# Optimization experiments

Hardware: AMD Instinct MI355X
Metric: run time of the kernel (lower is better)

The kernel has to match this reference:

```python
import jax, jax.numpy as jnp
import numpy as np

D_IN = 1024
D_OUT = 1024
N_HEADS = 16
HEAD_DIM = D_OUT // N_HEADS


def setup_inputs() -> dict:
    key = jax.random.key(0)
    ks = jax.random.split(key, 5)
    scale = 0.02
    x = jax.random.normal(ks[0], (2, 2048, D_IN), dtype=jnp.float32)
    Wq = jax.random.normal(ks[1], (D_IN, D_OUT), dtype=jnp.float32) * scale
    Wk = jax.random.normal(ks[2], (D_IN, D_OUT), dtype=jnp.float32) * scale
    Wv = jax.random.normal(ks[3], (D_IN, D_OUT), dtype=jnp.float32) * scale
    Wout = jax.random.normal(ks[4], (D_OUT, D_OUT), dtype=jnp.float32) * scale
    return {"x": x, "Wq": Wq, "Wk": Wk, "Wv": Wv, "Wout": Wout}


def reference(x, Wq, Wk, Wv, Wout):
    batch, seq_len, _ = x.shape
    # projections (no bias)
    Q = (x @ Wq).reshape(batch, seq_len, N_HEADS, HEAD_DIM)
    K = (x @ Wk).reshape(batch, seq_len, N_HEADS, HEAD_DIM)
    V = (x @ Wv).reshape(batch, seq_len, N_HEADS, HEAD_DIM)
    # scores: [batch, heads, seq, seq]
    scores = jnp.einsum("bqhd,bkhd->bhqk", Q, K) / jnp.sqrt(
        jnp.asarray(HEAD_DIM, dtype=x.dtype)
    )
    # causal mask: positions k > q masked to -inf
    causal = jnp.tril(jnp.ones((seq_len, seq_len), dtype=bool))
    scores = jnp.where(causal[None, None], scores, -jnp.inf)
    weights = jax.nn.softmax(scores, axis=-1)
    vectors = jnp.einsum("bhqk,bkhd->bqhd", weights, V)
    vectors = vectors.reshape(batch, seq_len, D_OUT)
    return vectors @ Wout
```

## Files before the change

### kernel.cpp

```cpp
#include <hip/hip_runtime.h>
#include <hip/hip_bf16.h>


typedef __attribute__((ext_vector_type(8))) _Float16 vhalf8;
typedef __attribute__((ext_vector_type(4))) _Float16 vhalf4;
typedef __attribute__((ext_vector_type(4))) float vfloat4;

#define D_MODEL 1024
#define SEQ     2048
#define NB      2
#define NH      16
#define HD      64

#define SCALE_K1 0.18033688f

__device__ __forceinline__ void async16(const void* g, void* l) {
  __builtin_amdgcn_global_load_lds(
      (const __attribute__((address_space(1))) unsigned int*)g,
      (__attribute__((address_space(3))) unsigned int*)l, 16, 0, 0);
}

__global__ __launch_bounds__(256) void prep(
    const float* __restrict__ x,
    const float* __restrict__ Wq, const float* __restrict__ Wk,
    const float* __restrict__ Wv, const float* __restrict__ Wo,
    _Float16* __restrict__ Xh, _Float16* __restrict__ Wt_qkv,
    _Float16* __restrict__ Wot) {
  int z = blockIdx.z;
  int t = threadIdx.x;
  if (z == 4) {
    int id = blockIdx.y * 16 + blockIdx.x;
#pragma unroll
    for (int pass = 0; pass < 8; pass++) {
      size_t i = ((size_t)(pass * 256 + id) * 256 + t) * 8;
      float4 a = *(const float4*)&x[i];
      float4 b = *(const float4*)&x[i + 4];
      vhalf8 h;
      h[0] = (_Float16)a.x; h[1] = (_Float16)a.y;
      h[2] = (_Float16)a.z; h[3] = (_Float16)a.w;
      h[4] = (_Float16)b.x; h[5] = (_Float16)b.y;
      h[6] = (_Float16)b.z; h[7] = (_Float16)b.w;
      *(vhalf8*)&Xh[i] = h;
    }
    return;
  }
  __shared__ _Float16 tile[64][65];
  const float* in = (z == 0) ? Wq : (z == 1) ? Wk : (z == 2) ? Wv : Wo;
  _Float16* out = (z < 3) ? (Wt_qkv + (size_t)z * 1024 * 1024) : Wot;
  int c0 = blockIdx.x * 64, r0 = blockIdx.y * 64;
  int tc = t & 63, tr = t >> 6;
#pragma unroll
  for (int p = 0; p < 16; p++) {
    int r = tr + p * 4;
    tile[r][tc] = (_Float16)in[(size_t)(r0 + r) * 1024 + c0 + tc];
  }
  __syncthreads();
#pragma unroll
  for (int p = 0; p < 16; p++) {
    int r = tr + p * 4;
    out[(size_t)(c0 + r) * 1024 + r0 + tc] = tile[tc][r];
  }
}

template <int BN>
__global__ __launch_bounds__(256) void gemm128(
    const _Float16* __restrict__ A, const _Float16* __restrict__ Bt,
    _Float16* __restrict__ Ch, float* __restrict__ Cf,
    _Float16* __restrict__ Vt, int M, int N, int K, int mode) {
  constexpr int NC = 8 + BN / 16;
  constexpr int CPW = NC / 4;
  constexpr int JN = BN / 32;
  __shared__ _Float16 As[128 * 32];
  __shared__ _Float16 Bs[BN * 32];
  int m0 = blockIdx.x * 128, n0 = blockIdx.y * BN;
  int t = threadIdx.x;
  int lane = t & 63, wave = t >> 6;
  int wm = (wave >> 1) * 64, wn = (wave & 1) * (BN / 2);
  int col = lane & 15, quad = lane >> 4;
  int srow = lane >> 2;
  int skc = (lane & 3) << 3;

  vfloat4 acc[4][JN];
#pragma unroll
  for (int i = 0; i < 4; i++)
#pragma unroll
    for (int j = 0; j < JN; j++) {
      acc[i][j][0] = 0.f; acc[i][j][1] = 0.f;
      acc[i][j][2] = 0.f; acc[i][j][3] = 0.f;
    }

  for (int k0 = 0; k0 < K; k0 += 32) {
    __syncthreads();
#pragma unroll
    for (int j = 0; j < CPW; j++) {
      int c = wave * CPW + j;
      int row = ((c < 8) ? c : (c - 8)) * 16 + srow;
      if (c < 8)
        async16(&A[(size_t)(m0 + row) * K + k0 + skc], &As[c * 512]);
      else
        async16(&Bt[(size_t)(n0 + row) * K + k0 + skc], &Bs[(c - 8) * 512]);
    }
    __syncthreads();

    vhalf8 af[4], bf[JN];
#pragma unroll
    for (int i = 0; i < 4; i++)
      af[i] = *(const vhalf8*)&As[(wm + i * 16 + col) * 32 + quad * 8];
#pragma unroll
    for (int j = 0; j < JN; j++)
      bf[j] = *(const vhalf8*)&Bs[(wn + j * 16 + col) * 32 + quad * 8];
#pragma unroll
    for (int i = 0; i < 4; i++)
#pragma unroll
      for (int j = 0; j < JN; j++)
        acc[i][j] = __builtin_amdgcn_mfma_f32_16x16x32_f16(af[i], bf[j], acc[i][j], 0, 0, 0);
  }

  bool vmode = (mode == 2) && (n0 >= 2048);
#pragma unroll
  for (int i = 0; i < 4; i++)
#pragma unroll
    for (int j = 0; j < JN; j++)
#pragma unroll
      for (int r = 0; r < 4; r++) {
        int m = m0 + wm + i * 16 + quad * 4 + r;
        int n = n0 + wn + j * 16 + col;
        if (mode == 1) {
          Cf[(size_t)m * N + n] = acc[i][j][r];
        } else if (vmode) {
          int nn = n - 2048;
          int hh = nn >> 6, dd = nn & 63;
          int bb = m >> 11, ss = m & 2047;
          Vt[(((size_t)bb * NH + hh) * HD + dd) * SEQ + ss] = (_Float16)acc[i][j][r];
        } else {
          Ch[(size_t)m * N + n] = (_Float16)acc[i][j][r];
        }
      }
}

__global__ __launch_bounds__(512) void attn(
    const _Float16* __restrict__ QKV, const _Float16* __restrict__ Vt,
    _Float16* __restrict__ Vec) {
  int blk = blockIdx.x;
  int qt = 15 - (blk >> 5);
  int hb = blk & 31;
  int h = hb & 15;
  int b = hb >> 4;
  int q0 = qt * 128;

  const _Float16* Qb  = QKV + (size_t)(b * SEQ) * 3072 + h * HD;
  const _Float16* Kb  = QKV + (size_t)(b * SEQ) * 3072 + 1024 + h * HD;
  const _Float16* Vtb = Vt + (size_t)(b * NH + h) * HD * SEQ;

  int t = threadIdx.x;
  int lane = t & 63, wave = t >> 6;
  int col = lane & 15, quad = lane >> 4;
  int wq0 = q0 + wave * 16;

  __shared__ _Float16 Ks[64][72];
  __shared__ _Float16 Vs[64][72];
  __shared__ _Float16 Ps[8][16][72];

  vhalf8 qf0 = *(const vhalf8*)&Qb[(size_t)(wq0 + col) * 3072 + quad * 8];
  vhalf8 qf1 = *(const vhalf8*)&Qb[(size_t)(wq0 + col) * 3072 + 32 + quad * 8];
#pragma unroll
  for (int i = 0; i < 8; i++) {
    qf0[i] = qf0[i] * (_Float16)SCALE_K1;
    qf1[i] = qf1[i] * (_Float16)SCALE_K1;
  }

  vfloat4 o[4];
#pragma unroll
  for (int i = 0; i < 4; i++) { o[i][0]=0.f; o[i][1]=0.f; o[i][2]=0.f; o[i][3]=0.f; }
  float lsum[4] = {0.f, 0.f, 0.f, 0.f};

  int srow = t >> 3;
  int scol = (t & 7) * 8;
  int kslot = ((srow & 3) << 4) + (srow >> 2);
  int kcol = scol ^ ((srow & 3) << 4);

  vhalf8 kr, vr;
  kr = *(const vhalf8*)&Kb[(size_t)srow * 3072 + scol];
  vr = *(const vhalf8*)&Vtb[(size_t)srow * SEQ + scol];

  for (int kb = 0; kb <= q0 + 127; kb += 64) {
    *(vhalf8*)&Ks[kslot][kcol] = kr;
    *(vhalf8*)&Vs[srow][scol]  = vr;
    __syncthreads();

    if (kb < q0 + 64) {
      kr = *(const vhalf8*)&Kb[(size_t)(kb + 64 + srow) * 3072 + scol];
      vr = *(const vhalf8*)&Vtb[(size_t)srow * SEQ + kb + 64 + scol];
    }

    if (kb <= wq0 + 15) {
      vfloat4 s[4];
#pragma unroll
      for (int hh = 0; hh < 4; hh++) {
        int sw = hh << 4;
        vhalf8 kf0 = *(const vhalf8*)&Ks[hh * 16 + col][(quad * 8) ^ sw];
        vhalf8 kf1 = *(const vhalf8*)&Ks[hh * 16 + col][(32 + quad * 8) ^ sw];
        vfloat4 z; z[0]=0.f; z[1]=0.f; z[2]=0.f; z[3]=0.f;
        z = __builtin_amdgcn_mfma_f32_16x16x32_f16(qf0, kf0, z, 0, 0, 0);
        z = __builtin_amdgcn_mfma_f32_16x16x32_f16(qf1, kf1, z, 0, 0, 0);
        s[hh] = z;
      }
      bool diag = (kb + 63 > wq0);
#pragma unroll
      for (int r = 0; r < 4; r++) {
        int q = wq0 + quad * 4 + r;
        float p[4];
#pragma unroll
        for (int hh = 0; hh < 4; hh++) {
          float sc = s[hh][r];
          if (diag && (kb + 4 * col + hh > q)) sc = -1e30f;
          p[hh] = __builtin_exp2f(sc);
        }
        lsum[r] += (p[0] + p[1]) + (p[2] + p[3]);
        vhalf4 ph;
        ph[0] = (_Float16)p[0]; ph[1] = (_Float16)p[1];
        ph[2] = (_Float16)p[2]; ph[3] = (_Float16)p[3];
        *(vhalf4*)&Ps[wave][quad * 4 + r][4 * col] = ph;
      }
      __asm__ __volatile__("s_waitcnt lgkmcnt(0)" ::: "memory");
      vhalf8 pf0 = *(const vhalf8*)&Ps[wave][col][quad * 8];
      vhalf8 pf1 = *(const vhalf8*)&Ps[wave][col][32 + quad * 8];
#pragma unroll
      for (int tt = 0; tt < 4; tt++) {
        vhalf8 vf0 = *(const vhalf8*)&Vs[tt * 16 + col][quad * 8];
        vhalf8 vf1 = *(const vhalf8*)&Vs[tt * 16 + col][32 + quad * 8];
        o[tt] = __builtin_amdgcn_mfma_f32_16x16x32_f16(pf0, vf0, o[tt], 0, 0, 0);
        o[tt] = __builtin_amdgcn_mfma_f32_16x16x32_f16(pf1, vf1, o[tt], 0, 0, 0);
      }
    }
    __syncthreads();
  }

  float inv_l[4];
#pragma unroll
  for (int r = 0; r < 4; r++) {
    float rs = lsum[r];
#pragma unroll
    for (int msk = 1; msk < 16; msk <<= 1) rs += __shfl_xor(rs, msk, 64);
    inv_l[r] = 1.0f / rs;
  }
#pragma unroll
  for (int tt = 0; tt < 4; tt++)
#pragma unroll
    for (int r = 0; r < 4; r++) {
      int q = wq0 + quad * 4 + r;
      int d = tt * 16 + col;
      Vec[(size_t)(b * SEQ + q) * D_MODEL + h * HD + d] =
          (_Float16)(o[tt][r] * inv_l[r]);
    }
}

extern "C" void kernel_launch(void* const* d_in, const int* in_sizes, int n_in,
                              void* d_out, int out_size, void* d_ws, size_t ws_size,
                              hipStream_t stream) {
  const float* x  = (const float*)d_in[0];
  const float* Wq = (const float*)d_in[1];
  const float* Wk = (const float*)d_in[2];
  const float* Wv = (const float*)d_in[3];
  const float* Wo = (const float*)d_in[4];
  float* out = (float*)d_out;

  char* ws = (char*)d_ws;
  _Float16* Xh     = (_Float16*)ws;
  _Float16* Wt_qkv = (_Float16*)(ws + 8388608);
  _Float16* Wot    = (_Float16*)(ws + 14680064);
  _Float16* QKV    = (_Float16*)(ws + 16777216);
  _Float16* Vt     = (_Float16*)(ws + 41943040);
  _Float16* Vec    = (_Float16*)(ws + 50331648);

  dim3 tb(256);
  prep<<<dim3(16, 16, 5), tb, 0, stream>>>(x, Wq, Wk, Wv, Wo, Xh, Wt_qkv, Wot);
  gemm128<128><<<dim3(32, 24), tb, 0, stream>>>(Xh, Wt_qkv, QKV, nullptr, Vt,
                                                4096, 3072, 1024, 2);
  attn<<<dim3(512), dim3(512), 0, stream>>>(QKV, Vt, Vec);
  gemm128<64><<<dim3(32, 16), tb, 0, stream>>>(Vec, Wot, nullptr, out, nullptr,
                                               4096, 1024, 1024, 1);
}
```

Measured before the change: 193.1 us.

## Double GEMM K-tile and give each attention wave two query groups

The GEMM kernel is templated on BK and now stages 64-wide K slices into shared memory, halving the number of barrier pairs per K loop. The attention kernel drops to 256 threads, with each wave handling 32 query rows as two 16-row groups. Each K/V fragment read from shared memory is reused across both groups, and each thread loads twice as many K/V elements per tile. The query-tile order is changed to interleave long and short causal tiles for load balance, at the cost of more registers per thread and fewer waves per block.

```diff
diff --git a/kernel.cpp b/kernel.cpp
--- a/kernel.cpp
+++ b/kernel.cpp
@@ -62,23 +62,26 @@
   }
 }
 
-template <int BN>
+template <int BN, int BK>
 __global__ __launch_bounds__(256) void gemm128(
     const _Float16* __restrict__ A, const _Float16* __restrict__ Bt,
     _Float16* __restrict__ Ch, float* __restrict__ Cf,
     _Float16* __restrict__ Vt, int M, int N, int K, int mode) {
-  constexpr int NC = 8 + BN / 16;
-  constexpr int CPW = NC / 4;
+  constexpr int ACH = 128 * BK / 512;
+  constexpr int BCH = BN * BK / 512;
+  constexpr int CPW = (ACH + BCH) / 4;
+  constexpr int RPC = 512 / BK;
+  constexpr int LPR = BK / 8;
   constexpr int JN = BN / 32;
-  __shared__ _Float16 As[128 * 32];
-  __shared__ _Float16 Bs[BN * 32];
+  __shared__ _Float16 As[128 * BK];
+  __shared__ _Float16 Bs[BN * BK];
   int m0 = blockIdx.x * 128, n0 = blockIdx.y * BN;
   int t = threadIdx.x;
   int lane = t & 63, wave = t >> 6;
   int wm = (wave >> 1) * 64, wn = (wave & 1) * (BN / 2);
   int col = lane & 15, quad = lane >> 4;
-  int srow = lane >> 2;
-  int skc = (lane & 3) << 3;
+  int srow = lane / LPR;
+  int skc = (lane % LPR) * 8;
 
   vfloat4 acc[4][JN];
 #pragma unroll
@@ -89,31 +92,36 @@
       acc[i][j][2] = 0.f; acc[i][j][3] = 0.f;
     }
 
-  for (int k0 = 0; k0 < K; k0 += 32) {
+  for (int k0 = 0; k0 < K; k0 += BK) {
     __syncthreads();
 #pragma unroll
     for (int j = 0; j < CPW; j++) {
       int c = wave * CPW + j;
-      int row = ((c < 8) ? c : (c - 8)) * 16 + srow;
-      if (c < 8)
+      if (c < ACH) {
+        int row = c * RPC + srow;
         async16(&A[(size_t)(m0 + row) * K + k0 + skc], &As[c * 512]);
-      else
-        async16(&Bt[(size_t)(n0 + row) * K + k0 + skc], &Bs[(c - 8) * 512]);
+      } else {
+        int row = (c - ACH) * RPC + srow;
+        async16(&Bt[(size_t)(n0 + row) * K + k0 + skc], &Bs[(c - ACH) * 512]);
+      }
     }
     __syncthreads();
 
-    vhalf8 af[4], bf[JN];
-#pragma unroll
-    for (int i = 0; i < 4; i++)
-      af[i] = *(const vhalf8*)&As[(wm + i * 16 + col) * 32 + quad * 8];
-#pragma unroll
-    for (int j = 0; j < JN; j++)
-      bf[j] = *(const vhalf8*)&Bs[(wn + j * 16 + col) * 32 + quad * 8];
-#pragma unroll
-    for (int i = 0; i < 4; i++)
+#pragma unroll
+    for (int sub = 0; sub < BK / 32; sub++) {
+      vhalf8 af[4], bf[JN];
+#pragma unroll
+      for (int i = 0; i < 4; i++)
+        af[i] = *(const vhalf8*)&As[(wm + i * 16 + col) * BK + sub * 32 + quad * 8];
 #pragma unroll
       for (int j = 0; j < JN; j++)
-        acc[i][j] = __builtin_amdgcn_mfma_f32_16x16x32_f16(af[i], bf[j], acc[i][j], 0, 0, 0);
+        bf[j] = *(const vhalf8*)&Bs[(wn + j * 16 + col) * BK + sub * 32 + quad * 8];
+#pragma unroll
+      for (int i = 0; i < 4; i++)
+#pragma unroll
+        for (int j = 0; j < JN; j++)
+          acc[i][j] = __builtin_amdgcn_mfma_f32_16x16x32_f16(af[i], bf[j], acc[i][j], 0, 0, 0);
+    }
   }
 
   bool vmode = (mode == 2) && (n0 >= 2048);
@@ -138,11 +146,12 @@
       }
 }
 
-__global__ __launch_bounds__(512) void attn(
+__global__ __launch_bounds__(256) void attn(
     const _Float16* __restrict__ QKV, const _Float16* __restrict__ Vt,
     _Float16* __restrict__ Vec) {
   int blk = blockIdx.x;
-  int qt = 15 - (blk >> 5);
+  int j = blk >> 5;
+  int qt = (j < 8) ? (15 - j) : (j - 8);
   int hb = blk & 31;
   int h = hb & 15;
   int b = hb >> 4;
@@ -155,104 +164,137 @@
   int t = threadIdx.x;
   int lane = t & 63, wave = t >> 6;
   int col = lane & 15, quad = lane >> 4;
-  int wq0 = q0 + wave * 16;
+  int wq0 = q0 + wave * 32;
 
   __shared__ _Float16 Ks[64][72];
   __shared__ _Float16 Vs[64][72];
-  __shared__ _Float16 Ps[8][16][72];
-
-  vhalf8 qf0 = *(const vhalf8*)&Qb[(size_t)(wq0 + col) * 3072 + quad * 8];
-  vhalf8 qf1 = *(const vhalf8*)&Qb[(size_t)(wq0 + col) * 3072 + 32 + quad * 8];
-#pragma unroll
-  for (int i = 0; i < 8; i++) {
-    qf0[i] = qf0[i] * (_Float16)SCALE_K1;
-    qf1[i] = qf1[i] * (_Float16)SCALE_K1;
-  }
-
-  vfloat4 o[4];
-#pragma unroll
-  for (int i = 0; i < 4; i++) { o[i][0]=0.f; o[i][1]=0.f; o[i][2]=0.f; o[i][3]=0.f; }
-  float lsum[4] = {0.f, 0.f, 0.f, 0.f};
-
-  int srow = t >> 3;
-  int scol = (t & 7) * 8;
+  __shared__ _Float16 Ps[4][32][72];
+
+  vhalf8 qf[2][2];
+#pragma unroll
+  for (int g = 0; g < 2; g++) {
+    qf[g][0] = *(const vhalf8*)&Qb[(size_t)(wq0 + g * 16 + col) * 3072 + quad * 8];
+    qf[g][1] = *(const vhalf8*)&Qb[(size_t)(wq0 + g * 16 + col) * 3072 + 32 + quad * 8];
+#pragma unroll
+    for (int i = 0; i < 8; i++) {
+      qf[g][0][i] = qf[g][0][i] * (_Float16)SCALE_K1;
+      qf[g][1][i] = qf[g][1][i] * (_Float16)SCALE_K1;
+    }
+  }
+
+  vfloat4 o[2][4];
+#pragma unroll
+  for (int g = 0; g < 2; g++)
+#pragma unroll
+    for (int i = 0; i < 4; i++) {
+      o[g][i][0] = 0.f; o[g][i][1] = 0.f; o[g][i][2] = 0.f; o[g][i][3] = 0.f;
+    }
+  float lsum[2][4] = {{0.f, 0.f, 0.f, 0.f}, {0.f, 0.f, 0.f, 0.f}};
+
+  int srow = t >> 2;
+  int scol = (t & 3) * 16;
   int kslot = ((srow & 3) << 4) + (srow >> 2);
   int kcol = scol ^ ((srow & 3) << 4);
 
-  vhalf8 kr, vr;
-  kr = *(const vhalf8*)&Kb[(size_t)srow * 3072 + scol];
-  vr = *(const vhalf8*)&Vtb[(size_t)srow * SEQ + scol];
+  vhalf8 kr0, kr1, vr0, vr1;
+  {
+    const _Float16* kg = &Kb[(size_t)srow * 3072 + scol];
+    kr0 = *(const vhalf8*)kg; kr1 = *(const vhalf8*)(kg + 8);
+    const _Float16* vg = &Vtb[(size_t)srow * SEQ + scol];
+    vr0 = *(const vhalf8*)vg; vr1 = *(const vhalf8*)(vg + 8);
+  }
 
   for (int kb = 0; kb <= q0 + 127; kb += 64) {
-    *(vhalf8*)&Ks[kslot][kcol] = kr;
-    *(vhalf8*)&Vs[srow][scol]  = vr;
+    *(vhalf8*)&Ks[kslot][kcol]     = kr0;
+    *(vhalf8*)&Ks[kslot][kcol + 8] = kr1;
+    *(vhalf8*)&Vs[srow][scol]      = vr0;
+    *(vhalf8*)&Vs[srow][scol + 8]  = vr1;
     __syncthreads();
 
     if (kb < q0 + 64) {
-      kr = *(const vhalf8*)&Kb[(size_t)(kb + 64 + srow) * 3072 + scol];
-      vr = *(const vhalf8*)&Vtb[(size_t)srow * SEQ + kb + 64 + scol];
-    }
-
-    if (kb <= wq0 + 15) {
-      vfloat4 s[4];
+      const _Float16* kg = &Kb[(size_t)(kb + 64 + srow) * 3072 + scol];
+      kr0 = *(const vhalf8*)kg; kr1 = *(const vhalf8*)(kg + 8);
+      const _Float16* vg = &Vtb[(size_t)srow * SEQ + kb + 64 + scol];
+      vr0 = *(const vhalf8*)vg; vr1 = *(const vhalf8*)(vg + 8);
+    }
+
+    if (kb <= wq0 + 31) {
+      vhalf8 kf[4][2];
 #pragma unroll
       for (int hh = 0; hh < 4; hh++) {
         int sw = hh << 4;
-        vhalf8 kf0 = *(const vhalf8*)&Ks[hh * 16 + col][(quad * 8) ^ sw];
-        vhalf8 kf1 = *(const vhalf8*)&Ks[hh * 16 + col][(32 + quad * 8) ^ sw];
-        vfloat4 z; z[0]=0.f; z[1]=0.f; z[2]=0.f; z[3]=0.f;
-        z = __builtin_amdgcn_mfma_f32_16x16x32_f16(qf0, kf0, z, 0, 0, 0);
-        z = __builtin_amdgcn_mfma_f32_16x16x32_f16(qf1, kf1, z, 0, 0, 0);
-        s[hh] = z;
-      }
-      bool diag = (kb + 63 > wq0);
+        kf[hh][0] = *(const vhalf8*)&Ks[hh * 16 + col][(quad * 8) ^ sw];
+        kf[hh][1] = *(const vhalf8*)&Ks[hh * 16 + col][(32 + quad * 8) ^ sw];
+      }
+#pragma unroll
+      for (int g = 0; g < 2; g++) {
+        vfloat4 s[4];
+#pragma unroll
+        for (int hh = 0; hh < 4; hh++) {
+          vfloat4 z; z[0]=0.f; z[1]=0.f; z[2]=0.f; z[3]=0.f;
+          z = __builtin_amdgcn_mfma_f32_16x16x32_f16(qf[g][0], kf[hh][0], z, 0, 0, 0);
+          z = __builtin_amdgcn_mfma_f32_16x16x32_f16(qf[g][1], kf[hh][1], z, 0, 0, 0);
+          s[hh] = z;
+        }
+        bool diag = (kb + 63 > wq0 + g * 16);
+#pragma unroll
+        for (int r = 0; r < 4; r++) {
+          int q = wq0 + g * 16 + quad * 4 + r;
+          float p[4];
+#pragma unroll
+          for (int hh = 0; hh < 4; hh++) {
+            float sc = s[hh][r];
+            if (diag && (kb + 4 * col + hh > q)) sc = -1e30f;
+            p[hh] = __builtin_exp2f(sc);
+          }
+          lsum[g][r] += (p[0] + p[1]) + (p[2] + p[3]);
+          vhalf4 ph;
+          ph[0] = (_Float16)p[0]; ph[1] = (_Float16)p[1];
+          ph[2] = (_Float16)p[2]; ph[3] = (_Float16)p[3];
+          *(vhalf4*)&Ps[wave][g * 16 + quad * 4 + r][4 * col] = ph;
+        }
+      }
+      __asm__ __volatile__("s_waitcnt lgkmcnt(0)" ::: "memory");
+      vhalf8 vf[4][2];
+#pragma unroll
+      for (int tt = 0; tt < 4; tt++) {
+        vf[tt][0] = *(const vhalf8*)&Vs[tt * 16 + col][quad * 8];
+        vf[tt][1] = *(const vhalf8*)&Vs[tt * 16 + col][32 + quad * 8];
+      }
+#pragma unroll
+      for (int g = 0; g < 2; g++) {
+        vhalf8 pf0 = *(const vhalf8*)&Ps[wave][g * 16 + col][quad * 8];
+        vhalf8 pf1 = *(const vhalf8*)&Ps[wave][g * 16 + col][32 + quad * 8];
+#pragma unroll
+        for (int tt = 0; tt < 4; tt++) {
+          o[g][tt] = __builtin_amdgcn_mfma_f32_16x16x32_f16(pf0, vf[tt][0], o[g][tt], 0, 0, 0);
+          o[g][tt] = __builtin_amdgcn_mfma_f32_16x16x32_f16(pf1, vf[tt][1], o[g][tt], 0, 0, 0);
+        }
+      }
+    }
+    __syncthreads();
+  }
+
+#pragma unroll
+  for (int g = 0; g < 2; g++) {
+    float inv_l[4];
+#pragma unroll
+    for (int r = 0; r < 4; r++) {
+      float rs = lsum[g][r];
+#pragma unroll
+      for (int msk = 1; msk < 16; msk <<= 1) rs += __shfl_xor(rs, msk, 64);
+      inv_l[r] = 1.0f / rs;
+    }
+#pragma unroll
+    for (int tt = 0; tt < 4; tt++)
 #pragma unroll
       for (int r = 0; r < 4; r++) {
-        int q = wq0 + quad * 4 + r;
-        float p[4];
-#pragma unroll
-        for (int hh = 0; hh < 4; hh++) {
-          float sc = s[hh][r];
-          if (diag && (kb + 4 * col + hh > q)) sc = -1e30f;
-          p[hh] = __builtin_exp2f(sc);
-        }
-        lsum[r] += (p[0] + p[1]) + (p[2] + p[3]);
-        vhalf4 ph;
-        ph[0] = (_Float16)p[0]; ph[1] = (_Float16)p[1];
-        ph[2] = (_Float16)p[2]; ph[3] = (_Float16)p[3];
-        *(vhalf4*)&Ps[wave][quad * 4 + r][4 * col] = ph;
-      }
-      __asm__ __volatile__("s_waitcnt lgkmcnt(0)" ::: "memory");
-      vhalf8 pf0 = *(const vhalf8*)&Ps[wave][col][quad * 8];
-      vhalf8 pf1 = *(const vhalf8*)&Ps[wave][col][32 + quad * 8];
-#pragma unroll
-      for (int tt = 0; tt < 4; tt++) {
-        vhalf8 vf0 = *(const vhalf8*)&Vs[tt * 16 + col][quad * 8];
-        vhalf8 vf1 = *(const vhalf8*)&Vs[tt * 16 + col][32 + quad * 8];
-        o[tt] = __builtin_amdgcn_mfma_f32_16x16x32_f16(pf0, vf0, o[tt], 0, 0, 0);
-        o[tt] = __builtin_amdgcn_mfma_f32_16x16x32_f16(pf1, vf1, o[tt], 0, 0, 0);
-      }
-    }
-    __syncthreads();
-  }
-
-  float inv_l[4];
-#pragma unroll
-  for (int r = 0; r < 4; r++) {
-    float rs = lsum[r];
-#pragma unroll
-    for (int msk = 1; msk < 16; msk <<= 1) rs += __shfl_xor(rs, msk, 64);
-    inv_l[r] = 1.0f / rs;
-  }
-#pragma unroll
-  for (int tt = 0; tt < 4; tt++)
-#pragma unroll
-    for (int r = 0; r < 4; r++) {
-      int q = wq0 + quad * 4 + r;
-      int d = tt * 16 + col;
-      Vec[(size_t)(b * SEQ + q) * D_MODEL + h * HD + d] =
-          (_Float16)(o[tt][r] * inv_l[r]);
-    }
+        int q = wq0 + g * 16 + quad * 4 + r;
+        int d = tt * 16 + col;
+        Vec[(size_t)(b * SEQ + q) * D_MODEL + h * HD + d] =
+            (_Float16)(o[g][tt][r] * inv_l[r]);
+      }
+  }
 }
 
 extern "C" void kernel_launch(void* const* d_in, const int* in_sizes, int n_in,
@@ -275,9 +317,9 @@
 
   dim3 tb(256);
   prep<<<dim3(16, 16, 5), tb, 0, stream>>>(x, Wq, Wk, Wv, Wo, Xh, Wt_qkv, Wot);
-  gemm128<128><<<dim3(32, 24), tb, 0, stream>>>(Xh, Wt_qkv, QKV, nullptr, Vt,
-                                                4096, 3072, 1024, 2);
-  attn<<<dim3(512), dim3(512), 0, stream>>>(QKV, Vt, Vec);
-  gemm128<64><<<dim3(32, 16), tb, 0, stream>>>(Vec, Wot, nullptr, out, nullptr,
-                                               4096, 1024, 1024, 1);
-}
+  gemm128<128, 64><<<dim3(32, 24), tb, 0, stream>>>(Xh, Wt_qkv, QKV, nullptr, Vt,
+                                                    4096, 3072, 1024, 2);
+  attn<<<dim3(512), tb, 0, stream>>>(QKV, Vt, Vec);
+  gemm128<64, 64><<<dim3(32, 16), tb, 0, stream>>>(Vec, Wot, nullptr, out, nullptr,
+                                                   4096, 1024, 1024, 1);
+}
```

Result: slower. 228.1 us (+18.2%).

## Pair causal attention tiles per block and swizzle GEMM LDS layout

Applied to the files above, without the earlier changes.

The attention kernel now uses 256-thread blocks that each handle two 64-row query tiles (tile pp and tile 31-pp). This balances causal work across blocks and prefetches the first K/V tile of the second phase while the first phase finishes. The GEMM applies an XOR swizzle to the global source column for async LDS loads and to the fragment reads, aiming to cut LDS bank conflicts. The cost is that each attention block serialises two passes with fewer waves per block.

```diff
diff --git a/kernel.cpp b/kernel.cpp
--- a/kernel.cpp
+++ b/kernel.cpp
@@ -67,8 +67,9 @@
     const _Float16* __restrict__ A, const _Float16* __restrict__ Bt,
     _Float16* __restrict__ Ch, float* __restrict__ Cf,
     _Float16* __restrict__ Vt, int M, int N, int K, int mode) {
-  constexpr int NC = 8 + BN / 16;
-  constexpr int CPW = NC / 4;
+  constexpr int ACH = 8;
+  constexpr int BCH = BN / 16;
+  constexpr int CPW = (ACH + BCH) / 4;
   constexpr int JN = BN / 32;
   __shared__ _Float16 As[128 * 32];
   __shared__ _Float16 Bs[BN * 32];
@@ -78,7 +79,7 @@
   int wm = (wave >> 1) * 64, wn = (wave & 1) * (BN / 2);
   int col = lane & 15, quad = lane >> 4;
   int srow = lane >> 2;
-  int skc = (lane & 3) << 3;
+  int gcol = (((lane & 3) ^ (srow & 3)) << 3);
 
   vfloat4 acc[4][JN];
 #pragma unroll
@@ -89,26 +90,30 @@
       acc[i][j][2] = 0.f; acc[i][j][3] = 0.f;
     }
 
+  int xq = (quad ^ (col & 3)) * 8;
+
   for (int k0 = 0; k0 < K; k0 += 32) {
     __syncthreads();
 #pragma unroll
     for (int j = 0; j < CPW; j++) {
       int c = wave * CPW + j;
-      int row = ((c < 8) ? c : (c - 8)) * 16 + srow;
-      if (c < 8)
-        async16(&A[(size_t)(m0 + row) * K + k0 + skc], &As[c * 512]);
-      else
-        async16(&Bt[(size_t)(n0 + row) * K + k0 + skc], &Bs[(c - 8) * 512]);
+      if (c < ACH) {
+        int row = c * 16 + srow;
+        async16(&A[(size_t)(m0 + row) * K + k0 + gcol], &As[c * 512]);
+      } else {
+        int row = (c - ACH) * 16 + srow;
+        async16(&Bt[(size_t)(n0 + row) * K + k0 + gcol], &Bs[(c - ACH) * 512]);
+      }
     }
     __syncthreads();
 
     vhalf8 af[4], bf[JN];
 #pragma unroll
     for (int i = 0; i < 4; i++)
-      af[i] = *(const vhalf8*)&As[(wm + i * 16 + col) * 32 + quad * 8];
+      af[i] = *(const vhalf8*)&As[(wm + i * 16 + col) * 32 + xq];
 #pragma unroll
     for (int j = 0; j < JN; j++)
-      bf[j] = *(const vhalf8*)&Bs[(wn + j * 16 + col) * 32 + quad * 8];
+      bf[j] = *(const vhalf8*)&Bs[(wn + j * 16 + col) * 32 + xq];
 #pragma unroll
     for (int i = 0; i < 4; i++)
 #pragma unroll
@@ -138,15 +143,14 @@
       }
 }
 
-__global__ __launch_bounds__(512) void attn(
+__global__ __launch_bounds__(256) void attn(
     const _Float16* __restrict__ QKV, const _Float16* __restrict__ Vt,
     _Float16* __restrict__ Vec) {
   int blk = blockIdx.x;
-  int qt = 15 - (blk >> 5);
+  int pp = blk >> 5;
   int hb = blk & 31;
   int h = hb & 15;
   int b = hb >> 4;
-  int q0 = qt * 128;
 
   const _Float16* Qb  = QKV + (size_t)(b * SEQ) * 3072 + h * HD;
   const _Float16* Kb  = QKV + (size_t)(b * SEQ) * 3072 + 1024 + h * HD;
@@ -155,54 +159,72 @@
   int t = threadIdx.x;
   int lane = t & 63, wave = t >> 6;
   int col = lane & 15, quad = lane >> 4;
-  int wq0 = q0 + wave * 16;
 
   __shared__ _Float16 Ks[64][72];
   __shared__ _Float16 Vs[64][72];
-  __shared__ _Float16 Ps[8][16][72];
-
-  vhalf8 qf0 = *(const vhalf8*)&Qb[(size_t)(wq0 + col) * 3072 + quad * 8];
-  vhalf8 qf1 = *(const vhalf8*)&Qb[(size_t)(wq0 + col) * 3072 + 32 + quad * 8];
-#pragma unroll
-  for (int i = 0; i < 8; i++) {
-    qf0[i] = qf0[i] * (_Float16)SCALE_K1;
-    qf1[i] = qf1[i] * (_Float16)SCALE_K1;
-  }
-
-  vfloat4 o[4];
-#pragma unroll
-  for (int i = 0; i < 4; i++) { o[i][0]=0.f; o[i][1]=0.f; o[i][2]=0.f; o[i][3]=0.f; }
-  float lsum[4] = {0.f, 0.f, 0.f, 0.f};
-
-  int srow = t >> 3;
-  int scol = (t & 7) * 8;
+  __shared__ _Float16 Ps[4][16][72];
+
+  int srow = t >> 2;
+  int scol = (t & 3) * 16;
   int kslot = ((srow & 3) << 4) + (srow >> 2);
   int kcol = scol ^ ((srow & 3) << 4);
 
-  vhalf8 kr, vr;
-  kr = *(const vhalf8*)&Kb[(size_t)srow * 3072 + scol];
-  vr = *(const vhalf8*)&Vtb[(size_t)srow * SEQ + scol];
-
-  for (int kb = 0; kb <= q0 + 127; kb += 64) {
-    *(vhalf8*)&Ks[kslot][kcol] = kr;
-    *(vhalf8*)&Vs[srow][scol]  = vr;
-    __syncthreads();
-
-    if (kb < q0 + 64) {
-      kr = *(const vhalf8*)&Kb[(size_t)(kb + 64 + srow) * 3072 + scol];
-      vr = *(const vhalf8*)&Vtb[(size_t)srow * SEQ + kb + 64 + scol];
-    }
-
-    if (kb <= wq0 + 15) {
-      vfloat4 s[4];
+  int tiles[2] = {31 - pp, pp};
+
+  vhalf8 kr0, kr1, vr0, vr1;
+  {
+    const _Float16* kg = &Kb[(size_t)srow * 3072 + scol];
+    kr0 = *(const vhalf8*)kg; kr1 = *(const vhalf8*)(kg + 8);
+    const _Float16* vg = &Vtb[(size_t)srow * SEQ + scol];
+    vr0 = *(const vhalf8*)vg; vr1 = *(const vhalf8*)(vg + 8);
+  }
+
+#pragma unroll
+  for (int phase = 0; phase < 2; phase++) {
+    int q0 = tiles[phase] * 64;
+    int wq0 = q0 + wave * 16;
+
+    vhalf8 qf0 = *(const vhalf8*)&Qb[(size_t)(wq0 + col) * 3072 + quad * 8];
+    vhalf8 qf1 = *(const vhalf8*)&Qb[(size_t)(wq0 + col) * 3072 + 32 + quad * 8];
+#pragma unroll
+    for (int i = 0; i < 8; i++) {
+      qf0[i] = qf0[i] * (_Float16)SCALE_K1;
+      qf1[i] = qf1[i] * (_Float16)SCALE_K1;
+    }
+
+    vfloat4 o[4];
+#pragma unroll
+    for (int i = 0; i < 4; i++) { o[i][0]=0.f; o[i][1]=0.f; o[i][2]=0.f; o[i][3]=0.f; }
+    float lsum[4] = {0.f, 0.f, 0.f, 0.f};
+
+    for (int kb = 0; kb <= q0; kb += 64) {
+      *(vhalf8*)&Ks[kslot][kcol]     = kr0;
+      *(vhalf8*)&Ks[kslot][kcol + 8] = kr1;
+      *(vhalf8*)&Vs[srow][scol]      = vr0;
+      *(vhalf8*)&Vs[srow][scol + 8]  = vr1;
+      __syncthreads();
+
+      int nxt = (kb < q0) ? (kb + 64) : ((phase == 0) ? 0 : -1);
+      if (nxt >= 0) {
+        const _Float16* kg = &Kb[(size_t)(nxt + srow) * 3072 + scol];
+        kr0 = *(const vhalf8*)kg; kr1 = *(const vhalf8*)(kg + 8);
+        const _Float16* vg = &Vtb[(size_t)srow * SEQ + nxt + scol];
+        vr0 = *(const vhalf8*)vg; vr1 = *(const vhalf8*)(vg + 8);
+      }
+
+      vhalf8 kf[4][2];
 #pragma unroll
       for (int hh = 0; hh < 4; hh++) {
         int sw = hh << 4;
-        vhalf8 kf0 = *(const vhalf8*)&Ks[hh * 16 + col][(quad * 8) ^ sw];
-        vhalf8 kf1 = *(const vhalf8*)&Ks[hh * 16 + col][(32 + quad * 8) ^ sw];
+        kf[hh][0] = *(const vhalf8*)&Ks[hh * 16 + col][(quad * 8) ^ sw];
+        kf[hh][1] = *(const vhalf8*)&Ks[hh * 16 + col][(32 + quad * 8) ^ sw];
+      }
+      vfloat4 s[4];
+#pragma unroll
+      for (int hh = 0; hh < 4; hh++) {
         vfloat4 z; z[0]=0.f; z[1]=0.f; z[2]=0.f; z[3]=0.f;
-        z = __builtin_amdgcn_mfma_f32_16x16x32_f16(qf0, kf0, z, 0, 0, 0);
-        z = __builtin_amdgcn_mfma_f32_16x16x32_f16(qf1, kf1, z, 0, 0, 0);
+        z = __builtin_amdgcn_mfma_f32_16x16x32_f16(qf0, kf[hh][0], z, 0, 0, 0);
+        z = __builtin_amdgcn_mfma_f32_16x16x32_f16(qf1, kf[hh][1], z, 0, 0, 0);
         s[hh] = z;
       }
       bool diag = (kb + 63 > wq0);
@@ -232,27 +254,27 @@
         o[tt] = __builtin_amdgcn_mfma_f32_16x16x32_f16(pf0, vf0, o[tt], 0, 0, 0);
         o[tt] = __builtin_amdgcn_mfma_f32_16x16x32_f16(pf1, vf1, o[tt], 0, 0, 0);
       }
-    }
-    __syncthreads();
-  }
-
-  float inv_l[4];
-#pragma unroll
-  for (int r = 0; r < 4; r++) {
-    float rs = lsum[r];
-#pragma unroll
-    for (int msk = 1; msk < 16; msk <<= 1) rs += __shfl_xor(rs, msk, 64);
-    inv_l[r] = 1.0f / rs;
-  }
-#pragma unroll
-  for (int tt = 0; tt < 4; tt++)
+      __syncthreads();
+    }
+
+    float inv_l[4];
 #pragma unroll
     for (int r = 0; r < 4; r++) {
-      int q = wq0 + quad * 4 + r;
-      int d = tt * 16 + col;
-      Vec[(size_t)(b * SEQ + q) * D_MODEL + h * HD + d] =
-          (_Float16)(o[tt][r] * inv_l[r]);
-    }
+      float rs = lsum[r];
+#pragma unroll
+      for (int msk = 1; msk < 16; msk <<= 1) rs += __shfl_xor(rs, msk, 64);
+      inv_l[r] = 1.0f / rs;
+    }
+#pragma unroll
+    for (int tt = 0; tt < 4; tt++)
+#pragma unroll
+      for (int r = 0; r < 4; r++) {
+        int q = wq0 + quad * 4 + r;
+        int d = tt * 16 + col;
+        Vec[(size_t)(b * SEQ + q) * D_MODEL + h * HD + d] =
+            (_Float16)(o[tt][r] * inv_l[r]);
+      }
+  }
 }
 
 extern "C" void kernel_launch(void* const* d_in, const int* in_sizes, int n_in,
@@ -277,7 +299,7 @@
   prep<<<dim3(16, 16, 5), tb, 0, stream>>>(x, Wq, Wk, Wv, Wo, Xh, Wt_qkv, Wot);
   gemm128<128><<<dim3(32, 24), tb, 0, stream>>>(Xh, Wt_qkv, QKV, nullptr, Vt,
                                                 4096, 3072, 1024, 2);
-  attn<<<dim3(512), dim3(512), 0, stream>>>(QKV, Vt, Vec);
+  attn<<<dim3(512), tb, 0, stream>>>(QKV, Vt, Vec);
   gemm128<64><<<dim3(32, 16), tb, 0, stream>>>(Vec, Wot, nullptr, out, nullptr,
                                                4096, 1024, 1024, 1);
 }
```

After: 192.7 us. About the same (-0.2%).
